# Kernel tuning notes

Measured on AMD Instinct MI355X. Metric: run time of the kernel, lower is better.

The kernel has to match this reference:

```python
import jax, jax.numpy as jnp
import numpy as np


def _direction(x, W_in, conv_w, conv_b, W_xproj, A_log, D, W_out):
    # x: [b, l, d_model]
    b, L, _ = x.shape
    d_inner = A_log.shape[0]
    xz = x @ W_in.T                         # [b, l, 2*d_inner]
    xc, z = jnp.split(xz, 2, axis=-1)
    # depthwise causal conv1d (left pad d_conv-1, keep first L outputs)
    xt = jnp.transpose(xc, (0, 2, 1))       # [b, d_inner, l]
    k = conv_w.shape[-1]
    xt = jax.lax.conv_general_dilated(
        xt, conv_w, window_strides=(1,), padding=[(k - 1, 0)],
        dimension_numbers=("NCH", "OIH", "NCH"), feature_group_count=d_inner)
    xt = xt + conv_b[None, :, None]
    xc = jax.nn.silu(jnp.transpose(xt, (0, 2, 1)))  # [b, l, d_inner]
    proj = xc @ W_xproj.T                   # [b, l, d_inner + 2*n]
    n = (proj.shape[-1] - d_inner) // 2
    delta = jax.nn.softplus(proj[..., :d_inner])
    Bm = proj[..., d_inner:d_inner + n]
    Cm = proj[..., d_inner + n:]
    A = -jnp.exp(A_log)                     # [d_inner]

    def step(s, inp):
        u_t, dt, B_t, C_t = inp             # [b,d], [b,d], [b,n], [b,n]
        dA = jnp.exp(dt[..., None] * A[None, :, None])          # [b,d,n]
        s = dA * s + dt[..., None] * B_t[:, None, :] * u_t[..., None]
        y = jnp.einsum('bn,bdn->bd', C_t, s) + D * u_t
        return s, y

    s0 = jnp.zeros((b, d_inner, n), x.dtype)
    xs = (jnp.swapaxes(xc, 0, 1), jnp.swapaxes(delta, 0, 1),
          jnp.swapaxes(Bm, 0, 1), jnp.swapaxes(Cm, 0, 1))
    _, ys = jax.lax.scan(step, s0, xs)      # ys: [l, b, d_inner]
    y = jnp.swapaxes(ys, 0, 1)
    y = y * jax.nn.silu(z)
    return y @ W_out.T                      # [b, l, d_model]


def setup_inputs() -> dict:
    key = jax.random.key(0)
    ks = jax.random.split(key, 8)
    b, L, d_model, d_inner, n, k = 2, 1024, 512, 1024, 64, 4
    s = lambda kk, shape, sc=0.02: jax.random.normal(kk, shape, jnp.float32) * sc
    return {
        "x": jax.random.normal(ks[0], (b, L, d_model), jnp.float32),
        "W_in": s(ks[1], (2 * d_inner, d_model)),
        "conv_w": s(ks[2], (d_inner, 1, k), 0.1),
        "conv_b": s(ks[3], (d_inner,), 0.1),
        "W_xproj": s(ks[4], (d_inner + 2 * n, d_inner)),
        "A_log": jax.random.normal(ks[5], (d_inner,), jnp.float32),
        "D": jnp.ones((d_inner,), jnp.float32),
        "W_out": s(ks[6], (d_model, d_inner)),
    }


def reference(x, W_in, conv_w, conv_b, W_xproj, A_log, D, W_out):
    out_fwd = _direction(x, W_in, conv_w, conv_b, W_xproj, A_log, D, W_out)
    out_bwd = _direction(jnp.flip(x, axis=1), W_in, conv_w, conv_b, W_xproj, A_log, D, W_out)
    return 0.5 * (out_fwd + jnp.flip(out_bwd, axis=1))
```

## Files before the change

kernel.cpp:

```cpp
#include <hip/hip_runtime.h>
#include <math.h>

#define B_    2
#define LSEQ  1024
#define DM    512
#define DI    1024
#define NS    64
#define TC    64
#define NC    (LSEQ/TC)
#define LDP   72

typedef __bf16 bf16x8 __attribute__((ext_vector_type(8)));
typedef float  f32x4  __attribute__((ext_vector_type(4)));

__device__ __forceinline__ float sp_f(float x)   { return fmaxf(x, 0.f) + log1pf(expf(-fabsf(x))); }
__device__ __forceinline__ float silu_f(float x) { return x / (1.f + expf(-x)); }
__device__ __forceinline__ unsigned short f2bf(float f) {
    unsigned int u = __float_as_uint(f);
    u += 0x7FFF + ((u >> 16) & 1);
    return (unsigned short)(u >> 16);
}
__device__ __forceinline__ float bf2f(unsigned short h) {
    return __uint_as_float(((unsigned int)h) << 16);
}
__device__ __forceinline__ void gload16(const void* g, void* l) {
    __builtin_amdgcn_global_load_lds(
        (const __attribute__((address_space(1))) unsigned int*)g,
        (__attribute__((address_space(3))) unsigned int*)l, 16, 0, 0);
}

__global__ __launch_bounds__(256) void castall(
    const float* __restrict__ x, const float* __restrict__ W_in,
    const float* __restrict__ W_xproj, const float* __restrict__ W_out,
    unsigned short* __restrict__ xb, unsigned short* __restrict__ winb,
    unsigned short* __restrict__ wxb, unsigned short* __restrict__ wob)
{
    int i = (blockIdx.x * 256 + threadIdx.x) * 4;
    const float* s; unsigned short* dst; int off;
    if (i < 1048576)      { s = x;       dst = xb;   off = i; }
    else if (i < 2097152) { s = W_in;    dst = winb; off = i - 1048576; }
    else if (i < 3276800) { s = W_xproj; dst = wxb;  off = i - 2097152; }
    else                  { s = W_out;   dst = wob;  off = i - 3276800; }
    float4 v = *(const float4*)(s + off);
    ushort4 o;
    o.x = f2bf(v.x); o.y = f2bf(v.y); o.z = f2bf(v.z); o.w = f2bf(v.w);
    *(ushort4*)(dst + off) = o;
}

__global__ __launch_bounds__(256) void gemm128(
    const unsigned short* __restrict__ Alo, const unsigned short* __restrict__ Ahi,
    const unsigned short* __restrict__ B, float* __restrict__ C,
    int M, int N, int K, int wrapK, int ks, int mode,
    const float* __restrict__ A_log, const unsigned short* __restrict__ u_in,
    unsigned* __restrict__ ddu_out,
    unsigned short* __restrict__ Bbf, unsigned short* __restrict__ Cbf)
{
    __shared__ short As0[128 * 64];
    __shared__ short Bs0[64 * 64];
    __shared__ short As1[128 * 64];
    __shared__ short Bs1[64 * 64];
    const int tid  = threadIdx.x;
    const int lane = tid & 63, wid = tid >> 6;

    const int gx = gridDim.x;
    int id  = blockIdx.y * gx + blockIdx.x;
    int q   = (gx * gridDim.y) >> 3;
    int swz = (id & 7) * q + (id >> 3);
    const int bm = (swz / gx) * 128, bn = (swz % gx) * 64;

    const int wm = wid * 32;
    const int fr = lane & 15;
    const int h  = fr & 7;
    const int tq = lane >> 4;
    const int Kc = K / ks;
    const int k0beg = blockIdx.z * Kc;
    const int nsteps = Kc / 64;
    float* Cz = C + (size_t)blockIdx.z * M * N;
    unsigned short* Czb = (unsigned short*)C + (size_t)blockIdx.z * M * N;

    const unsigned short* Asrc;
    int ka0;
    if (k0beg >= wrapK) { Asrc = Ahi; ka0 = k0beg - wrapK; }
    else                { Asrc = Alo; ka0 = k0beg; }

    const char* pA[4];
    const char* pB[2];
#pragma unroll
    for (int r = 0; r < 4; r++) {
        int o    = tid * 16 + r * 4096;
        int row  = o >> 7;
        int colb = ((((o >> 4) & 7) ^ (row & 7)) << 4);
        pA[r] = (const char*)Asrc + ((size_t)(bm + row) * wrapK + ka0) * 2 + colb;
    }
#pragma unroll
    for (int r = 0; r < 2; r++) {
        int o    = tid * 16 + r * 4096;
        int row  = o >> 7;
        int colb = ((((o >> 4) & 7) ^ (row & 7)) << 4);
        pB[r] = (const char*)B + ((size_t)(bn + row) * wrapK + ka0) * 2 + colb;
    }
    const int wbase = wid * 1024;

    f32x4 acc[2][4];
#pragma unroll
    for (int i = 0; i < 2; i++)
#pragma unroll
        for (int j = 0; j < 4; j++) acc[i][j] = (f32x4)0.f;

    auto STAGE = [&](char* Adst, char* Bdst) {
#pragma unroll
        for (int r = 0; r < 4; r++) { gload16(pA[r], Adst + wbase + r * 4096); pA[r] += 128; }
#pragma unroll
        for (int r = 0; r < 2; r++) { gload16(pB[r], Bdst + wbase + r * 4096); pB[r] += 128; }
    };
    auto COMPUTE = [&](const short* Asrc_l, const short* Bsrc_l) {
#pragma unroll
        for (int kk = 0; kk < 2; kk++) {
            const int sc = ((kk * 4 + tq) ^ h) << 3;
            bf16x8 af[2], bfr[4];
#pragma unroll
            for (int i = 0; i < 2; i++)
                af[i] = *reinterpret_cast<const bf16x8*>(&Asrc_l[(wm + i * 16 + fr) * 64 + sc]);
#pragma unroll
            for (int j = 0; j < 4; j++)
                bfr[j] = *reinterpret_cast<const bf16x8*>(&Bsrc_l[(j * 16 + fr) * 64 + sc]);
#pragma unroll
            for (int i = 0; i < 2; i++)
#pragma unroll
                for (int j = 0; j < 4; j++)
                    acc[i][j] = __builtin_amdgcn_mfma_f32_16x16x32_bf16(af[i], bfr[j], acc[i][j], 0, 0, 0);
        }
    };

    STAGE((char*)As0, (char*)Bs0);
    __syncthreads();
    for (int st = 0; st < nsteps; st += 2) {
        if (st + 1 < nsteps) STAGE((char*)As1, (char*)Bs1);
        COMPUTE(As0, Bs0);
        __syncthreads();
        if (st + 1 < nsteps) {
            if (st + 2 < nsteps) STAGE((char*)As0, (char*)Bs0);
            COMPUTE(As1, Bs1);
            __syncthreads();
        }
    }

    const int crow = (lane >> 4) * 4;
    if (mode == 2) {
        if (bn < 1024) {
#pragma unroll
            for (int j = 0; j < 4; j++) {
                int d = bn + j * 16 + fr;
                float nAd = -expf(A_log[d]);
#pragma unroll
                for (int i = 0; i < 2; i++)
#pragma unroll
                    for (int r = 0; r < 4; r++) {
                        int m = bm + wm + i * 16 + crow + r;
                        float delta = sp_f(acc[i][j][r]);
                        size_t idx = (size_t)m * DI + d;
                        float dA = expf(delta * nAd);
                        float du = delta * bf2f(u_in[idx]);
                        ddu_out[idx] = (unsigned)f2bf(dA) | ((unsigned)f2bf(du) << 16);
                    }
            }
        } else {
#pragma unroll
            for (int j = 0; j < 4; j++) {
                int cc = bn + j * 16 + fr;
#pragma unroll
                for (int i = 0; i < 2; i++)
#pragma unroll
                    for (int r = 0; r < 4; r++) {
                        int m = bm + wm + i * 16 + crow + r;
                        unsigned short v16 = f2bf(acc[i][j][r]);
                        if (cc < 1024 + NS) Bbf[(size_t)m * NS + cc - 1024]      = v16;
                        else                Cbf[(size_t)m * NS + cc - 1024 - NS] = v16;
                    }
            }
        }
    } else {
#pragma unroll
        for (int i = 0; i < 2; i++)
#pragma unroll
            for (int j = 0; j < 4; j++)
#pragma unroll
                for (int r = 0; r < 4; r++) {
                    size_t idx = (size_t)(bm + wm + i * 16 + crow + r) * N + (bn + j * 16 + fr);
                    if (mode == 1) Czb[idx] = f2bf(acc[i][j][r]);
                    else           Cz[idx]  = acc[i][j][r];
                }
    }
}

__global__ __launch_bounds__(256) void reduce4(
    const float* __restrict__ p, float* __restrict__ out, int n)
{
    int i = (blockIdx.x * 256 + threadIdx.x) * 4;
    if (i >= n) return;
    float4 a = *(const float4*)(p + i);
    float4 b = *(const float4*)(p + n + i);
    float4 c = *(const float4*)(p + 2 * n + i);
    float4 d = *(const float4*)(p + 3 * n + i);
    float4 o;
    o.x = (a.x + b.x) + (c.x + d.x);
    o.y = (a.y + b.y) + (c.y + d.y);
    o.z = (a.z + b.z) + (c.z + d.z);
    o.w = (a.w + b.w) + (c.w + d.w);
    *(float4*)(out + i) = o;
}

__global__ __launch_bounds__(256) void convk(
    const unsigned short* __restrict__ xzb, const float* __restrict__ cw,
    const float* __restrict__ cb, const float* __restrict__ Dvec,
    unsigned short* __restrict__ uc2b, unsigned short* __restrict__ ygb,
    unsigned short* __restrict__ Fbuf)
{
    int idx = blockIdx.x * 256 + threadIdx.x;
    int b   = idx >> 20;
    int rem = idx & ((LSEQ * DI) - 1);
    int tau = rem >> 10;
    int d   = rem & (DI - 1);

    const unsigned short* xc = xzb + (size_t)b * LSEQ * (2 * DI);
    float w0 = cw[d * 4 + 0], w1 = cw[d * 4 + 1], w2 = cw[d * 4 + 2], w3 = cw[d * 4 + 3];
    float bias = cb[d];
    float accf = bias, accb = bias;
    {
        int t0 = tau - 3, t1 = tau - 2, t2 = tau - 1;
        if (t0 >= 0) accf = fmaf(w0, bf2f(xc[(size_t)t0 * 2048 + d]), accf);
        if (t1 >= 0) accf = fmaf(w1, bf2f(xc[(size_t)t1 * 2048 + d]), accf);
        if (t2 >= 0) accf = fmaf(w2, bf2f(xc[(size_t)t2 * 2048 + d]), accf);
        accf = fmaf(w3, bf2f(xc[(size_t)tau * 2048 + d]), accf);
    }
    {
        int t0 = tau + 3, t1 = tau + 2, t2 = tau + 1;
        if (t0 < LSEQ) accb = fmaf(w0, bf2f(xc[(size_t)t0 * 2048 + d]), accb);
        if (t1 < LSEQ) accb = fmaf(w1, bf2f(xc[(size_t)t1 * 2048 + d]), accb);
        if (t2 < LSEQ) accb = fmaf(w2, bf2f(xc[(size_t)t2 * 2048 + d]), accb);
        accb = fmaf(w3, bf2f(xc[(size_t)tau * 2048 + d]), accb);
    }
    float uf = silu_f(accf), ub = silu_f(accb);
    size_t fi = ((size_t)b * LSEQ + tau) * DI + d;
    size_t bi = ((size_t)(2 + b) * LSEQ + tau) * DI + d;
    uc2b[fi] = f2bf(uf);
    uc2b[bi] = f2bf(ub);
    float Dd = Dvec[d];
    ygb[fi] = f2bf(Dd * uf);
    ygb[bi] = f2bf(Dd * ub);
    float z = bf2f(xc[(size_t)tau * 2048 + DI + d]);
    Fbuf[fi] = f2bf(0.5f * silu_f(z));
}

__global__ __launch_bounds__(256) void passA(
    const unsigned* __restrict__ ddu,
    const unsigned short* __restrict__ Bbf, const unsigned short* __restrict__ Cbf,
    unsigned short* __restrict__ ygb, unsigned short* __restrict__ gbuf,
    unsigned short* __restrict__ sEnd, float* __restrict__ Pbuf)
{
    const int dl   = threadIdx.x >> 2;
    const int nq   = threadIdx.x & 3;
    const int d0   = blockIdx.x * 64;
    const int d    = d0 + dl;
    const int c    = blockIdx.y;
    const int dirb = blockIdx.z;
    const int dir  = dirb >> 1;

    __shared__ float Bsh[TC][NS];
    __shared__ float Csh[TC][NS];
    __shared__ unsigned short gshY[TC][64];
    __shared__ unsigned short gshG[TC][64];

    for (int i = threadIdx.x * 4; i < TC * NS; i += 1024) {
        int tl = i >> 6, n = i & 63;
        int tau = dir ? (LSEQ - 1 - (c * TC + tl)) : (c * TC + tl);
        ushort4 vb = *(const ushort4*)&Bbf[((size_t)dirb * LSEQ + tau) * NS + n];
        ushort4 vc = *(const ushort4*)&Cbf[((size_t)dirb * LSEQ + tau) * NS + n];
        Bsh[tl][n+0] = bf2f(vb.x); Bsh[tl][n+1] = bf2f(vb.y);
        Bsh[tl][n+2] = bf2f(vb.z); Bsh[tl][n+3] = bf2f(vb.w);
        Csh[tl][n+0] = bf2f(vc.x); Csh[tl][n+1] = bf2f(vc.y);
        Csh[tl][n+2] = bf2f(vc.z); Csh[tl][n+3] = bf2f(vc.w);
    }
    __syncthreads();

    float s[16];
#pragma unroll
    for (int i = 0; i < 16; i++) s[i] = 0.f;
    float g_run = 1.f;

    int tau0 = dir ? (LSEQ - 1 - c * TC) : (c * TC);
    long stp = (dir ? -1L : 1L) * (long)DI;
    const unsigned* pW = ddu + ((size_t)dirb * LSEQ + tau0) * DI + d;
    const unsigned short* pY = ygb + ((size_t)dirb * LSEQ + tau0) * DI + d;

    unsigned w = *pW;
    float Du = bf2f(*pY);
    for (int tl = 0; tl < TC; tl++) {
        unsigned w_c = w;
        float Du_c = Du;
        if (tl + 1 < TC) {
            pW += stp; pY += stp;
            w = *pW; Du = bf2f(*pY);
        }
        float dA_c = bf2f((unsigned short)(w_c & 0xffff));
        float du_c = bf2f((unsigned short)(w_c >> 16));
        g_run *= dA_c;
        float ydot = 0.f;
        const float4* brow = (const float4*)&Bsh[tl][nq * 16];
        const float4* crow = (const float4*)&Csh[tl][nq * 16];
#pragma unroll
        for (int q = 0; q < 4; q++) {
            float4 bv = brow[q];
            float4 cv = crow[q];
            float s0 = fmaf(du_c, bv.x, dA_c * s[4*q+0]); s[4*q+0] = s0; ydot = fmaf(cv.x, s0, ydot);
            float s1 = fmaf(du_c, bv.y, dA_c * s[4*q+1]); s[4*q+1] = s1; ydot = fmaf(cv.y, s1, ydot);
            float s2 = fmaf(du_c, bv.z, dA_c * s[4*q+2]); s[4*q+2] = s2; ydot = fmaf(cv.z, s2, ydot);
            float s3 = fmaf(du_c, bv.w, dA_c * s[4*q+3]); s[4*q+3] = s3; ydot = fmaf(cv.w, s3, ydot);
        }
        ydot += __shfl_xor(ydot, 1);
        ydot += __shfl_xor(ydot, 2);
        if (nq == 0) {
            gshY[tl][dl] = f2bf(Du_c + ydot);
            gshG[tl][dl] = f2bf(g_run);
        }
    }
    __syncthreads();

    size_t base = (((size_t)dirb * NC + c) * DI + d) * NS + nq * 16;
#pragma unroll
    for (int q = 0; q < 4; q++) {
        ushort4 v;
        v.x = f2bf(s[4*q+0]); v.y = f2bf(s[4*q+1]);
        v.z = f2bf(s[4*q+2]); v.w = f2bf(s[4*q+3]);
        *(ushort4*)&sEnd[base + q * 4] = v;
    }
    if (nq == 0) Pbuf[((size_t)dirb * NC + c) * DI + d] = g_run;

    for (int i = threadIdx.x * 4; i < TC * 64; i += 1024) {
        int tl = i >> 6, col = i & 63;
        int tau = dir ? (LSEQ - 1 - (c * TC + tl)) : (c * TC + tl);
        *(ushort4*)&ygb[((size_t)dirb * LSEQ + tau) * DI + d0 + col]  = *(const ushort4*)&gshY[tl][col];
        *(ushort4*)&gbuf[((size_t)dirb * LSEQ + tau) * DI + d0 + col] = *(const ushort4*)&gshG[tl][col];
    }
}

__global__ __launch_bounds__(256) void passB(
    const unsigned short* __restrict__ sEnd, const float* __restrict__ Pbuf,
    unsigned short* __restrict__ sInitB)
{
    const int fl   = blockIdx.x * 256 + threadIdx.x;
    const int dirb = blockIdx.y;
    const int d    = fl >> 6;
    float run = 0.f;
    for (int c = 0; c < NC; c++) {
        size_t idx = ((size_t)(dirb * NC + c)) * (DI * NS) + fl;
        float tmp = bf2f(sEnd[idx]);
        sInitB[idx] = f2bf(run);
        float P = Pbuf[((size_t)dirb * NC + c) * DI + d];
        run = fmaf(P, run, tmp);
    }
}

__global__ __launch_bounds__(256) void corrK(
    const unsigned short* __restrict__ Cbf, const unsigned short* __restrict__ sInitB,
    const unsigned short* __restrict__ gbuf, const unsigned short* __restrict__ Fbuf,
    unsigned short* __restrict__ ygb)
{
    const int tid  = threadIdx.x;
    const int lane = tid & 63, wid = tid >> 6;
    const int d0   = blockIdx.x * 128;
    const int c    = blockIdx.y;
    const int dirb = blockIdx.z;
    const int dir  = dirb >> 1;
    const int b    = dirb & 1;
    const int fr = lane & 15, fk = (lane >> 4) * 8;
    const int wm = (wid >> 1) * 32, wn = (wid & 1) * 64;

    __shared__ short Cs[64 * LDP];
    __shared__ short Ss[128 * LDP];
    __shared__ float corrS[64 * 128];

    for (int i = tid * 4; i < 64 * 64; i += 1024) {
        int tl = i >> 6, n = i & 63;
        int tau = dir ? (LSEQ - 1 - (c * TC + tl)) : (c * TC + tl);
        *(ushort4*)&Cs[tl * LDP + n] = *(const ushort4*)&Cbf[((size_t)dirb * LSEQ + tau) * NS + n];
    }
    for (int i = tid * 4; i < 128 * 64; i += 1024) {
        int r = i >> 6, n = i & 63;
        *(ushort4*)&Ss[r * LDP + n] =
            *(const ushort4*)&sInitB[(((size_t)dirb * NC + c) * DI + d0 + r) * NS + n];
    }
    __syncthreads();

    f32x4 acc[2][4];
#pragma unroll
    for (int i = 0; i < 2; i++)
#pragma unroll
        for (int j = 0; j < 4; j++) acc[i][j] = (f32x4)0.f;

#pragma unroll
    for (int kk = 0; kk < 2; kk++) {
        bf16x8 af[2], bfr[4];
#pragma unroll
        for (int i = 0; i < 2; i++)
            af[i] = *reinterpret_cast<const bf16x8*>(&Cs[(wm + i * 16 + fr) * LDP + kk * 32 + fk]);
#pragma unroll
        for (int j = 0; j < 4; j++)
            bfr[j] = *reinterpret_cast<const bf16x8*>(&Ss[(wn + j * 16 + fr) * LDP + kk * 32 + fk]);
#pragma unroll
        for (int i = 0; i < 2; i++)
#pragma unroll
            for (int j = 0; j < 4; j++)
                acc[i][j] = __builtin_amdgcn_mfma_f32_16x16x32_bf16(af[i], bfr[j], acc[i][j], 0, 0, 0);
    }

    const int crow = (lane >> 4) * 4;
#pragma unroll
    for (int i = 0; i < 2; i++)
#pragma unroll
        for (int j = 0; j < 4; j++)
#pragma unroll
            for (int r = 0; r < 4; r++)
                corrS[(wm + i * 16 + crow + r) * 128 + (wn + j * 16 + fr)] = acc[i][j][r];
    __syncthreads();

    for (int i = tid * 4; i < 64 * 128; i += 1024) {
        int tl = i >> 7, col = i & 127;
        int tau = dir ? (LSEQ - 1 - (c * TC + tl)) : (c * TC + tl);
        size_t gi = ((size_t)dirb * LSEQ + tau) * DI + d0 + col;
        size_t fi = ((size_t)b    * LSEQ + tau) * DI + d0 + col;
        ushort4 g4 = *(const ushort4*)&gbuf[gi];
        ushort4 y4 = *(const ushort4*)&ygb[gi];
        ushort4 F4 = *(const ushort4*)&Fbuf[fi];
        const float* cr = &corrS[tl * 128 + col];
        ushort4 o;
        o.x = f2bf(bf2f(F4.x) * fmaf(bf2f(g4.x), cr[0], bf2f(y4.x)));
        o.y = f2bf(bf2f(F4.y) * fmaf(bf2f(g4.y), cr[1], bf2f(y4.y)));
        o.z = f2bf(bf2f(F4.z) * fmaf(bf2f(g4.z), cr[2], bf2f(y4.z)));
        o.w = f2bf(bf2f(F4.w) * fmaf(bf2f(g4.w), cr[3], bf2f(y4.w)));
        *(ushort4*)&ygb[gi] = o;
    }
}

extern "C" void kernel_launch(void* const* d_in, const int* in_sizes, int n_in,
                              void* d_out, int out_size, void* d_ws, size_t ws_size,
                              hipStream_t stream)
{
    const float* x      = (const float*)d_in[0];
    const float* W_in   = (const float*)d_in[1];
    const float* conv_w = (const float*)d_in[2];
    const float* conv_b = (const float*)d_in[3];
    const float* W_xprj = (const float*)d_in[4];
    const float* A_log  = (const float*)d_in[5];
    const float* Dvec   = (const float*)d_in[6];
    const float* W_out  = (const float*)d_in[7];
    float* out = (float*)d_out;

    float* ws = (float*)d_ws;
    unsigned*       ddu   = (unsigned*)ws;
    unsigned short* uc2b  = (unsigned short*)(ws + 4194304);
    unsigned short* xzb   = uc2b + 4194304;
    unsigned short* ygb   = xzb  + 4194304;
    unsigned short* gbuf  = ygb  + 4194304;
    unsigned short* Fbuf  = gbuf + 4194304;
    unsigned short* Bbf   = Fbuf + 2097152;
    unsigned short* Cbf   = Bbf  + 262144;
    unsigned short* wob   = Cbf  + 262144;
    float*          Pbuf  = (float*)(wob + 524288);
    unsigned short* xb     = (unsigned short*)ddu;
    unsigned short* winb   = xb + 1048576;
    unsigned short* wxb    = gbuf;
    unsigned short* sEnd   = xzb;
    unsigned short* sInitB = uc2b;
    float*          gpart  = (float*)ddu;

    castall<<<3712, 256, 0, stream>>>(x, W_in, W_xprj, W_out, xb, winb, wxb, wob);

    gemm128<<<dim3(32, 16), 256, 0, stream>>>(xb, nullptr, winb, (float*)xzb,
        B_ * LSEQ, 2 * DI, DM, DM, 1, 1, nullptr, nullptr, nullptr, nullptr, nullptr);

    convk<<<(B_ * LSEQ * DI) / 256, 256, 0, stream>>>(xzb, conv_w, conv_b, Dvec, uc2b, ygb, Fbuf);

    gemm128<<<dim3(18, 32), 256, 0, stream>>>(uc2b, nullptr, wxb, nullptr,
        4 * LSEQ, DI + 2 * NS, DI, DI, 1, 2, A_log, uc2b, ddu, Bbf, Cbf);

    passA<<<dim3(16, NC, 4), 256, 0, stream>>>(ddu, Bbf, Cbf, ygb, gbuf, sEnd, Pbuf);

    passB<<<dim3(256, 4), 256, 0, stream>>>(sEnd, Pbuf, sInitB);

    corrK<<<dim3(8, NC, 4), 256, 0, stream>>>(Cbf, sInitB, gbuf, Fbuf, ygb);

    gemm128<<<dim3(8, 16, 4), 256, 0, stream>>>(ygb, ygb + (size_t)2 * LSEQ * DI, wob, gpart,
        B_ * LSEQ, DM, 2 * DI, DI, 4, 0, nullptr, nullptr, nullptr, nullptr, nullptr);
    reduce4<<<1024, 256, 0, stream>>>(gpart, out, B_ * LSEQ * DM);
}
```

Baseline: 144.6 us.

## Triple-buffer GEMM LDS staging with vmcnt waits and halve output split-K

Replaces the double-buffered LDS pipeline in the bf16 MFMA GEMM with a three-stage ring. Explicit s_waitcnt vmcnt plus a single s_barrier per step let two tile loads stay in flight while computing on the third. It also cuts the output projection's split-K from 4 to 2 and replaces the 4-way reduction with a 2-way one. LDS use per block rises to 72KB, which may lower occupancy, and the reduced split-K gives the final GEMM half as many blocks.

Result: no change. 145.3 us (+0.5%).

```diff
diff --git a/kernel.cpp b/kernel.cpp
--- a/kernel.cpp
+++ b/kernel.cpp
@@ -56,9 +56,11 @@
     unsigned short* __restrict__ Bbf, unsigned short* __restrict__ Cbf)
 {
     __shared__ short As0[128 * 64];
+    __shared__ short As1[128 * 64];
+    __shared__ short As2[128 * 64];
     __shared__ short Bs0[64 * 64];
-    __shared__ short As1[128 * 64];
     __shared__ short Bs1[64 * 64];
+    __shared__ short Bs2[64 * 64];
     const int tid  = threadIdx.x;
     const int lane = tid & 63, wid = tid >> 6;
 
@@ -107,11 +109,11 @@
 #pragma unroll
         for (int j = 0; j < 4; j++) acc[i][j] = (f32x4)0.f;
 
-    auto STAGE = [&](char* Adst, char* Bdst) {
-#pragma unroll
-        for (int r = 0; r < 4; r++) { gload16(pA[r], Adst + wbase + r * 4096); pA[r] += 128; }
-#pragma unroll
-        for (int r = 0; r < 2; r++) { gload16(pB[r], Bdst + wbase + r * 4096); pB[r] += 128; }
+    auto STAGE = [&](short* Adst, short* Bdst) {
+#pragma unroll
+        for (int r = 0; r < 4; r++) { gload16(pA[r], (char*)Adst + wbase + r * 4096); pA[r] += 128; }
+#pragma unroll
+        for (int r = 0; r < 2; r++) { gload16(pB[r], (char*)Bdst + wbase + r * 4096); pB[r] += 128; }
     };
     auto COMPUTE = [&](const short* Asrc_l, const short* Bsrc_l) {
 #pragma unroll
@@ -131,18 +133,25 @@
                     acc[i][j] = __builtin_amdgcn_mfma_f32_16x16x32_bf16(af[i], bfr[j], acc[i][j], 0, 0, 0);
         }
     };
-
-    STAGE((char*)As0, (char*)Bs0);
-    __syncthreads();
-    for (int st = 0; st < nsteps; st += 2) {
-        if (st + 1 < nsteps) STAGE((char*)As1, (char*)Bs1);
-        COMPUTE(As0, Bs0);
-        __syncthreads();
-        if (st + 1 < nsteps) {
-            if (st + 2 < nsteps) STAGE((char*)As0, (char*)Bs0);
-            COMPUTE(As1, Bs1);
-            __syncthreads();
+    auto STEP = [&](short* Acur, short* Bcur, short* Anxt, short* Bnxt, int t) {
+        if (t >= nsteps) return;
+        if (t + 2 < nsteps) {
+            asm volatile("s_waitcnt vmcnt(6)" ::: "memory");
+        } else {
+            asm volatile("s_waitcnt vmcnt(0)" ::: "memory");
         }
+        __builtin_amdgcn_sched_barrier(0);
+        __builtin_amdgcn_s_barrier();
+        COMPUTE(Acur, Bcur);
+        if (t + 2 < nsteps) STAGE(Anxt, Bnxt);
+    };
+
+    STAGE(As0, Bs0);
+    STAGE(As1, Bs1);
+    for (int t = 0; t < nsteps; t += 3) {
+        STEP(As0, Bs0, As2, Bs2, t);
+        STEP(As1, Bs1, As0, Bs0, t + 1);
+        STEP(As2, Bs2, As1, Bs1, t + 2);
     }
 
     const int crow = (lane >> 4) * 4;
@@ -193,20 +202,15 @@
     }
 }
 
-__global__ __launch_bounds__(256) void reduce4(
+__global__ __launch_bounds__(256) void reduce2(
     const float* __restrict__ p, float* __restrict__ out, int n)
 {
     int i = (blockIdx.x * 256 + threadIdx.x) * 4;
     if (i >= n) return;
     float4 a = *(const float4*)(p + i);
     float4 b = *(const float4*)(p + n + i);
-    float4 c = *(const float4*)(p + 2 * n + i);
-    float4 d = *(const float4*)(p + 3 * n + i);
     float4 o;
-    o.x = (a.x + b.x) + (c.x + d.x);
-    o.y = (a.y + b.y) + (c.y + d.y);
-    o.z = (a.z + b.z) + (c.z + d.z);
-    o.w = (a.w + b.w) + (c.w + d.w);
+    o.x = a.x + b.x; o.y = a.y + b.y; o.z = a.z + b.z; o.w = a.w + b.w;
     *(float4*)(out + i) = o;
 }
 
@@ -490,7 +494,7 @@
 
     corrK<<<dim3(8, NC, 4), 256, 0, stream>>>(Cbf, sInitB, gbuf, Fbuf, ygb);
 
-    gemm128<<<dim3(8, 16, 4), 256, 0, stream>>>(ygb, ygb + (size_t)2 * LSEQ * DI, wob, gpart,
-        B_ * LSEQ, DM, 2 * DI, DI, 4, 0, nullptr, nullptr, nullptr, nullptr, nullptr);
-    reduce4<<<1024, 256, 0, stream>>>(gpart, out, B_ * LSEQ * DM);
-}
+    gemm128<<<dim3(8, 16, 2), 256, 0, stream>>>(ygb, ygb + (size_t)2 * LSEQ * DI, wob, gpart,
+        B_ * LSEQ, DM, 2 * DI, DI, 2, 0, nullptr, nullptr, nullptr, nullptr, nullptr);
+    reduce2<<<1024, 256, 0, stream>>>(gpart, out, B_ * LSEQ * DM);
+}
```
